# Kernel optimization log

Measured on AMD Instinct MI355X. Metric: run time of the kernel, lower is better.

The kernel has to match this reference:

```python
import jax, jax.numpy as jnp
import numpy as np

DIM = 256
NUM_HEADS = 8
HEAD_DIM = DIM // NUM_HEADS
WINDOW = 256
STRIDE = 192  # int(256 * (1 - 0.25))
HIDDEN = int(DIM * 4.0)
EPS_IN = 1e-5


def setup_inputs() -> dict:
    key = jax.random.key(0)
    ks = jax.random.split(key, 10)
    B, C, L = 4, DIM, 8192
    s = lambda fan_in: 1.0 / np.sqrt(fan_in)
    return {
        "x": jax.random.normal(ks[0], (B, C, L), jnp.float32),
        "pos": jax.random.normal(ks[1], (1, C, 1), jnp.float32),
        "w_qkv": jax.random.normal(ks[2], (3 * C, C), jnp.float32) * s(C),
        "b_qkv": jax.random.normal(ks[3], (3 * C,), jnp.float32) * s(C),
        "w_out": jax.random.normal(ks[4], (C, C), jnp.float32) * s(C),
        "b_out": jax.random.normal(ks[5], (C,), jnp.float32) * s(C),
        "w_mlp1": jax.random.normal(ks[6], (HIDDEN, C), jnp.float32) * s(C),
        "b_mlp1": jax.random.normal(ks[7], (HIDDEN,), jnp.float32) * s(C),
        "w_mlp2": jax.random.normal(ks[8], (C, HIDDEN), jnp.float32) * s(HIDDEN),
        "b_mlp2": jax.random.normal(ks[9], (C,), jnp.float32) * s(HIDDEN),
    }


def conv1x1(x, w, b):
    # x: (B, Cin, L), w: (Cout, Cin), b: (Cout,)
    return jnp.einsum("oc,bcl->bol", w, x) + b[None, :, None]


def instance_norm(x, eps=EPS_IN):
    # InstanceNorm1d, affine=False: normalize each (B, C) row over L (biased var)
    mean = jnp.mean(x, axis=-1, keepdims=True)
    var = jnp.var(x, axis=-1, keepdims=True)
    return (x - mean) * jax.lax.rsqrt(var + eps)


def reference(x, pos, w_qkv, b_qkv, w_out, b_out, w_mlp1, b_mlp1, w_mlp2, b_mlp2):
    B, C, L = x.shape
    residual = x
    xp = x + pos
    qkv = conv1x1(xp, w_qkv, b_qkv)  # (B, 3C, L)
    q, k, v = jnp.split(qkv, 3, axis=1)
    # (B, H, L, hd)
    to_heads = lambda t: t.reshape(B, NUM_HEADS, HEAD_DIM, L).transpose(0, 1, 3, 2)
    q, k, v = to_heads(q), to_heads(k), to_heads(v)

    # static overlapping window index map
    starts = np.arange(0, L, STRIDE)                      # (nW,)
    idx = starts[:, None] + np.arange(WINDOW)[None, :]     # (nW, W)
    valid = idx < L                                        # (nW, W)
    idxc = np.minimum(idx, L - 1)
    valid_j = jnp.asarray(valid)

    qw = q[:, :, idxc, :]  # (B, H, nW, W, hd)
    kw = k[:, :, idxc, :]
    vw = v[:, :, idxc, :]
    scale = HEAD_DIM ** -0.5
    scores = jnp.einsum("bhnqd,bhnkd->bhnqk", qw, kw) * scale
    scores = jnp.where(valid_j[None, None, :, None, :], scores, -jnp.inf)
    attn = jax.nn.softmax(scores, axis=-1)
    win_out = jnp.einsum("bhnqk,bhnkd->bhnqd", attn, vw)
    win_out = win_out * valid_j[None, None, :, :, None]

    # overlap-add scatter + count normalization
    flat_idx = idxc.reshape(-1)
    out = jnp.zeros_like(q).at[:, :, flat_idx, :].add(
        win_out.reshape(B, NUM_HEADS, -1, HEAD_DIM))
    counts = jnp.zeros((L,), x.dtype).at[flat_idx].add(
        valid_j.reshape(-1).astype(x.dtype))
    out = out / jnp.clip(counts, 1e-8)[None, None, :, None]

    attn_out = out.transpose(0, 1, 3, 2).reshape(B, C, L)
    y = conv1x1(attn_out, w_out, b_out) + residual
    y = instance_norm(y)

    # AttentionMLP1D: conv1x1 -> GELU -> conv1x1 -> InstanceNorm, + residual
    h = jax.nn.gelu(conv1x1(y, w_mlp1, b_mlp1), approximate=False)
    m = instance_norm(conv1x1(h, w_mlp2, b_mlp2))
    return m + y
```

## Files before the change

### kernel.cpp

```cpp
#include <hip/hip_runtime.h>
#include <hip/hip_bf16.h>
#include <math.h>

#define B_   4
#define C_   256
#define L_   8192
#define NH   8
#define HD   32
#define WIN  256
#define STR  192
#define NWIN 43
#define HID  1024

typedef short short8 __attribute__((ext_vector_type(8)));
typedef float f32x4  __attribute__((ext_vector_type(4)));

typedef __attribute__((address_space(3))) unsigned int       as3_u32;
typedef __attribute__((address_space(1))) const unsigned int as1_u32;

__device__ __forceinline__ void gll16(const void* g, void* l) {
    __builtin_amdgcn_global_load_lds((as1_u32*)g, (as3_u32*)l, 16, 0, 0);
}

__device__ __forceinline__ short f2b(float f) {
    unsigned u = __builtin_bit_cast(unsigned, f);
    u += 0x7fffu + ((u >> 16) & 1u);
    return (short)(u >> 16);
}
__device__ __forceinline__ float b2f(short s) {
    return __builtin_bit_cast(float, (unsigned)((unsigned short)s) << 16);
}
__device__ __forceinline__ unsigned pk2(float a, float b) {
    return (unsigned)(unsigned short)f2b(a) | ((unsigned)(unsigned short)f2b(b) << 16);
}
__device__ __forceinline__ float gelu_exact(float v) {
    return 0.5f * v * (1.0f + erff(v * 0.70710678118654752f));
}

template<int MODE>
__global__ __launch_bounds__(256)
void mgemm(const short* __restrict__ Wb, const short* __restrict__ Xsrc,
           const float* __restrict__ bias, const float* __restrict__ resid,
           void* __restrict__ outp)
{
    constexpr int K = (MODE == 3) ? 1024 : 256;
    constexpr int M = (MODE == 0) ? 768 : (MODE == 2) ? 1024 : 256;
    constexpr int LDSZ = (MODE == 0 || MODE == 2) ? 34816 : 32768;
    __shared__ __align__(16) char lds[LDSZ];

    const int t    = threadIdx.x;
    const int lane = t & 63, wid = t >> 6;
    const int wm   = wid >> 1, wn = wid & 1;
    const int b    = blockIdx.z;
    const int o0   = blockIdx.y * 128;
    const int l0   = blockIdx.x * 128;
    const int l15  = lane & 15, kb = lane >> 4;

    f32x4 acc[4][4] = {};
    const short* Xb = Xsrc + (size_t)b * L_ * K;

    int pn1[4], pj1[4]; bool ptwo[4];
    if constexpr (MODE == 1) {
        #pragma unroll
        for (int it = 0; it < 4; ++it) {
            int r = (it * 256 + t) >> 3;
            int l = l0 + r;
            int n1 = l / STR;
            pn1[it] = n1; pj1[it] = l - n1 * STR;
            ptwo[it] = (n1 >= 1) && (pj1[it] < WIN - STR);
        }
    }

    for (int c0 = 0; c0 < K; c0 += 64) {
        __syncthreads();
        #pragma unroll
        for (int it = 0; it < 4; ++it) {
            int d = it * 256 + t;
            int r = d >> 3, pc = d & 7;
            int clog = pc ^ (r & 7);
            gll16(Wb + (size_t)(o0 + r) * K + c0 + clog * 8,
                  lds + (it * 256 + wid * 64) * 16);
        }
        if constexpr (MODE == 1) {
            #pragma unroll
            for (int it = 0; it < 4; ++it) {
                int d = it * 256 + t;
                int r = d >> 3, pc = d & 7;
                int clog = pc ^ (r & 7);
                int c = c0 + clog * 8;
                int h = c >> 5, dd = c & 31;
                size_t base = ((((size_t)(b * NH + h)) * NWIN + pn1[it]) * WIN + pj1[it]) * HD + dd;
                short8 vv = *(const short8*)&Xsrc[base];
                if (ptwo[it]) {
                    short8 u = *(const short8*)&Xsrc[base - 2048];
                    #pragma unroll
                    for (int e = 0; e < 8; ++e) vv[e] = f2b(b2f(vv[e]) + b2f(u[e]));
                }
                *(short8*)(lds + 16384 + d * 16) = vv;
            }
        } else {
            #pragma unroll
            for (int it = 0; it < 4; ++it) {
                int d = it * 256 + t;
                int r = d >> 3, pc = d & 7;
                int clog = pc ^ (r & 7);
                gll16(Xb + (size_t)(l0 + r) * K + c0 + clog * 8,
                      lds + 16384 + (it * 256 + wid * 64) * 16);
            }
        }
        __syncthreads();
        #pragma unroll
        for (int kk = 0; kk < 2; ++kk) {
            short8 af[4], bf[4];
            #pragma unroll
            for (int i = 0; i < 4; ++i)
                af[i] = *(const short8*)(lds +
                    ((wm * 64 + i * 16 + l15) * 8 + ((kk * 4 + kb) ^ (l15 & 7))) * 16);
            #pragma unroll
            for (int j = 0; j < 4; ++j)
                bf[j] = *(const short8*)(lds + 16384 +
                    ((wn * 64 + j * 16 + l15) * 8 + ((kk * 4 + kb) ^ (l15 & 7))) * 16);
            #pragma unroll
            for (int i = 0; i < 4; ++i)
                #pragma unroll
                for (int j = 0; j < 4; ++j)
                    acc[i][j] = __builtin_amdgcn_mfma_f32_16x16x32_bf16(af[i], bf[j], acc[i][j], 0, 0, 0);
        }
    }

    const int orow = (lane >> 4) * 4;

    if constexpr (MODE == 1 || MODE == 3) {
        float* out = (float*)outp;
        #pragma unroll
        for (int i = 0; i < 4; ++i) {
            #pragma unroll
            for (int r = 0; r < 4; ++r) {
                const int o = o0 + wm * 64 + i * 16 + orow + r;
                const float bv = bias[o];
                #pragma unroll
                for (int j = 0; j < 4; ++j) {
                    const int l = l0 + wn * 64 + j * 16 + l15;
                    float v = acc[i][j][r] + bv;
                    if (MODE == 1) v += resid[((size_t)b * C_ + o) * L_ + l];
                    out[((size_t)b * M + o) * L_ + l] = v;
                }
            }
        }
    } else {
        __syncthreads();
        short* Ts = (short*)lds;
        const float qscale = (MODE == 0 && o0 < 256) ? 0.17677669529663687f : 1.0f;
        #pragma unroll
        for (int i = 0; i < 4; ++i) {
            #pragma unroll
            for (int r = 0; r < 4; ++r) {
                const int ol = wm * 64 + i * 16 + orow + r;
                const float bv = bias[o0 + ol];
                #pragma unroll
                for (int j = 0; j < 4; ++j) {
                    const int ll = wn * 64 + j * 16 + l15;
                    float v = acc[i][j][r] + bv;
                    if (MODE == 2) v = gelu_exact(v);
                    if (MODE == 0) v *= qscale;
                    Ts[ll * 136 + ol] = f2b(v);
                }
            }
        }
        __syncthreads();
        if constexpr (MODE == 2) {
            short* ht = (short*)outp;
            #pragma unroll
            for (int it = 0; it < 8; ++it) {
                int idx = t + it * 256;
                int ll = idx >> 4, ck = (idx & 15) * 8;
                short8 v = *(const short8*)(Ts + ll * 136 + ck);
                *(short8*)(ht + ((size_t)b * L_ + l0 + ll) * HID + o0 + ck) = v;
            }
        } else {
            short* qkv = (short*)outp;
            #pragma unroll
            for (int it = 0; it < 8; ++it) {
                int idx = t + it * 256;
                int hb = idx >> 9, rem = idx & 511;
                int ll = rem >> 2, dk = (rem & 3) * 8;
                short8 v = *(const short8*)(Ts + ll * 136 + hb * 32 + dk);
                int og = o0 + hb * 32;
                int part = og >> 8, h = (og & 255) >> 5;
                short* dst = qkv + (size_t)part * ((size_t)B_ * NH * L_ * HD)
                           + (((size_t)(b * NH + h) * L_ + l0 + ll) * HD + dk);
                *(short8*)dst = v;
            }
        }
    }
}

__global__ __launch_bounds__(256)
void attn_k(const short* __restrict__ q, const short* __restrict__ k,
            const short* __restrict__ v, short* __restrict__ win_out)
{
    __shared__ __align__(16) short Kl[256][40];
    __shared__ __align__(16) short Vt[32][264];
    __shared__ __align__(16) short Pl[4][64][40];

    const int n = blockIdx.x, h = blockIdx.y, b = blockIdx.z;
    const int start = n * STR;
    const int t = threadIdx.x;
    const int lane = t & 63, w = t >> 6;
    const int l15 = lane & 15, kb = lane >> 4;
    const size_t hbase = (size_t)(b * NH + h) * L_ * HD;

    {
        int l = start + t; if (l > L_ - 1) l = L_ - 1;
        const short8* gk = (const short8*)&k[hbase + (size_t)l * HD];
        const short8* gv = (const short8*)&v[hbase + (size_t)l * HD];
        short8 k0 = gk[0], k1 = gk[1], k2 = gk[2], k3 = gk[3];
        short8 v0 = gv[0], v1 = gv[1], v2 = gv[2], v3 = gv[3];
        *(short8*)&Kl[t][0]  = k0; *(short8*)&Kl[t][8]  = k1;
        *(short8*)&Kl[t][16] = k2; *(short8*)&Kl[t][24] = k3;
        #pragma unroll
        for (int e = 0; e < 8; ++e) {
            Vt[e][t]      = v0[e];
            Vt[8 + e][t]  = v1[e];
            Vt[16 + e][t] = v2[e];
            Vt[24 + e][t] = v3[e];
        }
    }

    short8 qf[4];
    #pragma unroll
    for (int j = 0; j < 4; ++j) {
        int lq = start + w * 64 + j * 16 + l15; if (lq > L_ - 1) lq = L_ - 1;
        qf[j] = *(const short8*)&q[hbase + (size_t)lq * HD + kb * 8];
    }
    __syncthreads();

    const bool domask = (start + WIN > L_);
    f32x4 ot[2][4] = {};
    float ls[4] = {};
    const f32x4 zacc = {};

    for (int kt = 0; kt < 8; ++kt) {
        short8 ka[2];
        #pragma unroll
        for (int i = 0; i < 2; ++i)
            ka[i] = *(const short8*)&Kl[kt * 32 + i * 16 + l15][kb * 8];
        f32x4 st[2][4];
        #pragma unroll
        for (int i = 0; i < 2; ++i)
            #pragma unroll
            for (int j = 0; j < 4; ++j)
                st[i][j] = __builtin_amdgcn_mfma_f32_16x16x32_bf16(ka[i], qf[j], zacc, 0, 0, 0);

        if (domask) {
            #pragma unroll
            for (int i = 0; i < 2; ++i)
                #pragma unroll
                for (int r = 0; r < 4; ++r) {
                    int kp = start + kt * 32 + i * 16 + kb * 4 + r;
                    if (kp >= L_) {
                        #pragma unroll
                        for (int j = 0; j < 4; ++j) st[i][j][r] = -1e30f;
                    }
                }
        }

        #pragma unroll
        for (int j = 0; j < 4; ++j) {
            #pragma unroll
            for (int i = 0; i < 2; ++i) {
                float p0 = __expf(st[i][j][0]);
                float p1 = __expf(st[i][j][1]);
                float p2 = __expf(st[i][j][2]);
                float p3 = __expf(st[i][j][3]);
                ls[j] += (p0 + p1) + (p2 + p3);
                uint2 u;
                u.x = pk2(p0, p1);
                u.y = pk2(p2, p3);
                *(uint2*)&Pl[w][j * 16 + l15][i * 16 + kb * 4] = u;
            }
        }
        asm volatile("s_waitcnt lgkmcnt(0)" ::: "memory");
        __builtin_amdgcn_sched_barrier(0);

        short8 pb[4], va[2];
        #pragma unroll
        for (int j = 0; j < 4; ++j)
            pb[j] = *(const short8*)&Pl[w][j * 16 + l15][kb * 8];
        #pragma unroll
        for (int i = 0; i < 2; ++i)
            va[i] = *(const short8*)&Vt[i * 16 + l15][kt * 32 + kb * 8];
        #pragma unroll
        for (int i = 0; i < 2; ++i)
            #pragma unroll
            for (int j = 0; j < 4; ++j)
                ot[i][j] = __builtin_amdgcn_mfma_f32_16x16x32_bf16(va[i], pb[j], ot[i][j], 0, 0, 0);
    }

    float sc[4];
    #pragma unroll
    for (int j = 0; j < 4; ++j) {
        float s = ls[j];
        s += __shfl_xor(s, 16);
        s += __shfl_xor(s, 32);
        int lq = start + w * 64 + j * 16 + l15;
        int nhi = lq / STR;
        int nlo = (lq >= WIN) ? ((lq - WIN) / STR + 1) : 0;
        sc[j] = 1.0f / (s * (float)(nhi - nlo + 1));
    }

    short* base = win_out + (((size_t)(b * NH + h) * NWIN + n) * WIN) * HD;
    #pragma unroll
    for (int i = 0; i < 2; ++i)
        #pragma unroll
        for (int j = 0; j < 4; ++j) {
            int qrow = w * 64 + j * 16 + l15;
            int d    = i * 16 + kb * 4;
            f32x4 o = ot[i][j];
            uint2 u;
            u.x = pk2(o[0] * sc[j], o[1] * sc[j]);
            u.y = pk2(o[2] * sc[j], o[3] * sc[j]);
            *(uint2*)&base[(size_t)qrow * HD + d] = u;
        }
}

__global__ __launch_bounds__(256)
void stats_k(const float* __restrict__ src, float2* __restrict__ stt)
{
    const int row = blockIdx.x;
    const float* s = src + (size_t)row * L_;
    const int t = threadIdx.x;
    float sum = 0.f, ssq = 0.f;
    #pragma unroll
    for (int i = 0; i < 8; ++i) {
        float4 vv = *(const float4*)&s[t * 4 + i * 1024];
        sum += (vv.x + vv.y) + (vv.z + vv.w);
        ssq += vv.x*vv.x + vv.y*vv.y + vv.z*vv.z + vv.w*vv.w;
    }
    #pragma unroll
    for (int off = 32; off > 0; off >>= 1) {
        sum += __shfl_down(sum, off);
        ssq += __shfl_down(ssq, off);
    }
    __shared__ float rbuf[8];
    if ((t & 63) == 0) { rbuf[t >> 6] = sum; rbuf[4 + (t >> 6)] = ssq; }
    __syncthreads();
    if (t == 0) {
        float a  = (rbuf[0] + rbuf[1]) + (rbuf[2] + rbuf[3]);
        float q2 = (rbuf[4] + rbuf[5]) + (rbuf[6] + rbuf[7]);
        float mean = a * (1.0f / L_);
        float var  = q2 * (1.0f / L_) - mean * mean;
        stt[row] = make_float2(mean, rsqrtf(var + 1e-5f));
    }
}

__global__ __launch_bounds__(256)
void prep_k(const float* __restrict__ in, const float* __restrict__ pos,
            const float2* __restrict__ stt, short* __restrict__ outT)
{
    __shared__ float T[64][65];
    const int b = blockIdx.z, c0 = blockIdx.y * 64, l0 = blockIdx.x * 64;
    const int t = threadIdx.x;
    #pragma unroll
    for (int it = 0; it < 4; ++it) {
        int idx = t + it * 256;
        int c = idx >> 4, l4 = (idx & 15) * 4;
        float4 v = *(const float4*)&in[((size_t)b * C_ + c0 + c) * L_ + l0 + l4];
        if (stt) {
            float2 ms = stt[b * C_ + c0 + c];
            v.x = (v.x - ms.x) * ms.y; v.y = (v.y - ms.x) * ms.y;
            v.z = (v.z - ms.x) * ms.y; v.w = (v.w - ms.x) * ms.y;
        }
        float p = pos ? pos[c0 + c] : 0.f;
        T[c][l4 + 0] = v.x + p; T[c][l4 + 1] = v.y + p;
        T[c][l4 + 2] = v.z + p; T[c][l4 + 3] = v.w + p;
    }
    __syncthreads();
    #pragma unroll
    for (int it = 0; it < 2; ++it) {
        int idx = t + it * 256;
        int l = idx >> 3, ck = (idx & 7) * 8;
        short8 o;
        #pragma unroll
        for (int j = 0; j < 8; ++j) o[j] = f2b(T[ck + j][l]);
        *(short8*)&outT[((size_t)b * L_ + l0 + l) * C_ + c0 + ck] = o;
    }
}

__global__ __launch_bounds__(256)
void wconv_k(const float* a, const float* b, const float* c, const float* d,
             short* oa, short* ob, short* oc, short* od)
{
    int i = (blockIdx.x * 256 + threadIdx.x) * 8;
    const float* s; short* o; int off;
    if (i < 196608)      { s = a; o = oa; off = i; }
    else if (i < 262144) { s = b; o = ob; off = i - 196608; }
    else if (i < 524288) { s = c; o = oc; off = i - 262144; }
    else                 { s = d; o = od; off = i - 524288; }
    float4 v0 = *(const float4*)(s + off);
    float4 v1 = *(const float4*)(s + off + 4);
    short8 r;
    r[0] = f2b(v0.x); r[1] = f2b(v0.y); r[2] = f2b(v0.z); r[3] = f2b(v0.w);
    r[4] = f2b(v1.x); r[5] = f2b(v1.y); r[6] = f2b(v1.z); r[7] = f2b(v1.w);
    *(short8*)(o + off) = r;
}

__global__ __launch_bounds__(256)
void norm_k(const float* __restrict__ src, const float* __restrict__ add,
            const float2* __restrict__ ast, float* __restrict__ dst)
{
    const int row = blockIdx.x;
    const float* s = src + (size_t)row * L_;
    const int t = threadIdx.x;
    float4 vals[8];
    float sum = 0.f, ssq = 0.f;
    #pragma unroll
    for (int i = 0; i < 8; ++i) {
        float4 vv = *(const float4*)&s[t * 4 + i * 1024];
        vals[i] = vv;
        sum += (vv.x + vv.y) + (vv.z + vv.w);
        ssq += vv.x*vv.x + vv.y*vv.y + vv.z*vv.z + vv.w*vv.w;
    }
    #pragma unroll
    for (int off = 32; off > 0; off >>= 1) {
        sum += __shfl_down(sum, off);
        ssq += __shfl_down(ssq, off);
    }
    __shared__ float rbuf[8];
    __shared__ float s_mean, s_rstd;
    if ((t & 63) == 0) { rbuf[t >> 6] = sum; rbuf[4 + (t >> 6)] = ssq; }
    __syncthreads();
    if (t == 0) {
        float a  = (rbuf[0] + rbuf[1]) + (rbuf[2] + rbuf[3]);
        float q2 = (rbuf[4] + rbuf[5]) + (rbuf[6] + rbuf[7]);
        float mean = a * (1.0f / L_);
        float var  = q2 * (1.0f / L_) - mean * mean;
        s_mean = mean;
        s_rstd = rsqrtf(var + 1e-5f);
    }
    __syncthreads();
    const float mean = s_mean, rstd = s_rstd;
    const float2 ms = ast[row];
    float* d = dst + (size_t)row * L_;
    const float* ar = add + (size_t)row * L_;
    #pragma unroll
    for (int i = 0; i < 8; ++i) {
        float4 vv = vals[i];
        float4 av = *(const float4*)&ar[t * 4 + i * 1024];
        vv.x = (vv.x - mean) * rstd + (av.x - ms.x) * ms.y;
        vv.y = (vv.y - mean) * rstd + (av.y - ms.x) * ms.y;
        vv.z = (vv.z - mean) * rstd + (av.z - ms.x) * ms.y;
        vv.w = (vv.w - mean) * rstd + (av.w - ms.x) * ms.y;
        *(float4*)&d[t * 4 + i * 1024] = vv;
    }
}

extern "C" void kernel_launch(void* const* d_in, const int* in_sizes, int n_in,
                              void* d_out, int out_size, void* d_ws, size_t ws_size,
                              hipStream_t stream) {
    const float* x      = (const float*)d_in[0];
    const float* pos    = (const float*)d_in[1];
    const float* w_qkv  = (const float*)d_in[2];
    const float* b_qkv  = (const float*)d_in[3];
    const float* w_out  = (const float*)d_in[4];
    const float* b_out  = (const float*)d_in[5];
    const float* w_mlp1 = (const float*)d_in[6];
    const float* b_mlp1 = (const float*)d_in[7];
    const float* w_mlp2 = (const float*)d_in[8];
    const float* b_mlp2 = (const float*)d_in[9];
    float* out = (float*)d_out;

    constexpr size_t MB = 1u << 20;
    char* w = (char*)d_ws;
    short*  xp_t  = (short*)(w);
    short*  qb    = (short*)(w + 16 * MB);
    short*  winb  = (short*)(w + 64 * MB);
    float*  yb    = (float*)(w + 88 * MB);
    short*  y_t   = (short*)(w + 120 * MB);
    short*  h_t   = (short*)(w);
    float2* yst   = (float2*)(w + 136 * MB);
    short*  wqb   = (short*)(w + 137 * MB);
    short*  wob   = wqb + 196608;
    short*  wm1b  = wob + 65536;
    short*  wm2b  = wm1b + 262144;

    const size_t SZ = (size_t)B_ * C_ * L_;

    wconv_k<<<384, 256, 0, stream>>>(w_qkv, w_out, w_mlp1, w_mlp2, wqb, wob, wm1b, wm2b);
    prep_k <<<dim3(128, 4, B_), 256, 0, stream>>>(x, pos, nullptr, xp_t);

    mgemm<0><<<dim3(64, 6, B_), 256, 0, stream>>>(wqb, xp_t, b_qkv, nullptr, qb);
    attn_k  <<<dim3(NWIN, NH, B_), 256, 0, stream>>>(qb, qb + SZ, qb + 2 * SZ, winb);
    mgemm<1><<<dim3(64, 2, B_), 256, 0, stream>>>(wob, winb, b_out, x, yb);
    stats_k <<<B_ * C_, 256, 0, stream>>>(yb, yst);
    prep_k  <<<dim3(128, 4, B_), 256, 0, stream>>>(yb, nullptr, yst, y_t);
    mgemm<2><<<dim3(64, 8, B_), 256, 0, stream>>>(wm1b, y_t, b_mlp1, nullptr, h_t);
    mgemm<3><<<dim3(64, 2, B_), 256, 0, stream>>>(wm2b, h_t, b_mlp2, nullptr, out);
    norm_k  <<<B_ * C_, 256, 0, stream>>>(out, yb, yst, out);
}
```

Baseline: 205.3 us.

## Keep activation tile in registers and loop over output tiles with double-buffered weights

The GEMM kernel is restructured so that each block owns a 128-column L tile and keeps its activation operand in registers across all output-channel tiles. Weight tiles of 128x256 are streamed into a double-buffered 128 KB LDS area, with the next tile prefetched while MFMAs run. The grid shrinks to 64xB blocks with launch_bounds(256,1), trading parallelism and occupancy (only 256 blocks) for reuse of the activation operand. The exact erf GELU is also replaced by a tanh-style sigmoid approximation, which changes numerics slightly.

```diff
diff --git a/kernel.cpp b/kernel.cpp
--- a/kernel.cpp
+++ b/kernel.cpp
@@ -33,164 +33,171 @@
 __device__ __forceinline__ unsigned pk2(float a, float b) {
     return (unsigned)(unsigned short)f2b(a) | ((unsigned)(unsigned short)f2b(b) << 16);
 }
-__device__ __forceinline__ float gelu_exact(float v) {
-    return 0.5f * v * (1.0f + erff(v * 0.70710678118654752f));
+__device__ __forceinline__ float gelu_fast(float x) {
+    float t = x * x;
+    float u = fmaf(0.0713548162726f * t, x, 1.59576912161f * x);
+    return x * __frcp_rn(1.0f + __expf(-u));
 }
 
 template<int MODE>
-__global__ __launch_bounds__(256)
-void mgemm(const short* __restrict__ Wb, const short* __restrict__ Xsrc,
-           const float* __restrict__ bias, const float* __restrict__ resid,
-           void* __restrict__ outp)
+__global__ __launch_bounds__(256, 1)
+void wsg(const short* __restrict__ Wb, const short* __restrict__ Xsrc,
+         const float* __restrict__ bias, const float* __restrict__ resid,
+         void* __restrict__ outp)
 {
-    constexpr int K = (MODE == 3) ? 1024 : 256;
-    constexpr int M = (MODE == 0) ? 768 : (MODE == 2) ? 1024 : 256;
-    constexpr int LDSZ = (MODE == 0 || MODE == 2) ? 34816 : 32768;
-    __shared__ __align__(16) char lds[LDSZ];
+    constexpr int K   = (MODE == 3) ? 1024 : 256;
+    constexpr int M   = (MODE == 0) ? 768 : (MODE == 2) ? 1024 : 256;
+    constexpr int NOT = M / 128;
+    constexpr int NKO = K / 256;
+    constexpr int TOT = NOT * NKO;
+
+    __shared__ __align__(16) short lds[2][32768];
 
     const int t    = threadIdx.x;
     const int lane = t & 63, wid = t >> 6;
-    const int wm   = wid >> 1, wn = wid & 1;
-    const int b    = blockIdx.z;
-    const int o0   = blockIdx.y * 128;
+    const int wo   = wid >> 1, wl = wid & 1;
+    const int b    = blockIdx.y;
     const int l0   = blockIdx.x * 128;
     const int l15  = lane & 15, kb = lane >> 4;
-
-    f32x4 acc[4][4] = {};
-    const short* Xb = Xsrc + (size_t)b * L_ * K;
-
-    int pn1[4], pj1[4]; bool ptwo[4];
-    if constexpr (MODE == 1) {
-        #pragma unroll
-        for (int it = 0; it < 4; ++it) {
-            int r = (it * 256 + t) >> 3;
-            int l = l0 + r;
-            int n1 = l / STR;
-            pn1[it] = n1; pj1[it] = l - n1 * STR;
-            ptwo[it] = (n1 >= 1) && (pj1[it] < WIN - STR);
-        }
-    }
-
-    for (int c0 = 0; c0 < K; c0 += 64) {
-        __syncthreads();
-        #pragma unroll
-        for (int it = 0; it < 4; ++it) {
-            int d = it * 256 + t;
-            int r = d >> 3, pc = d & 7;
-            int clog = pc ^ (r & 7);
-            gll16(Wb + (size_t)(o0 + r) * K + c0 + clog * 8,
-                  lds + (it * 256 + wid * 64) * 16);
-        }
-        if constexpr (MODE == 1) {
-            #pragma unroll
-            for (int it = 0; it < 4; ++it) {
-                int d = it * 256 + t;
-                int r = d >> 3, pc = d & 7;
-                int clog = pc ^ (r & 7);
-                int c = c0 + clog * 8;
-                int h = c >> 5, dd = c & 31;
-                size_t base = ((((size_t)(b * NH + h)) * NWIN + pn1[it]) * WIN + pj1[it]) * HD + dd;
-                short8 vv = *(const short8*)&Xsrc[base];
-                if (ptwo[it]) {
-                    short8 u = *(const short8*)&Xsrc[base - 2048];
+    const int orow = kb * 4;
+
+    short8 bf[(MODE == 3) ? 2 : 1][4][8];
+
+    auto loadB = [&](short8 (*dst)[8], int ko) {
+        #pragma unroll
+        for (int j = 0; j < 4; ++j) {
+            const int l = l0 + wl * 64 + j * 16 + l15;
+            if constexpr (MODE == 1) {
+                const int n1 = l / STR, j1 = l - (l / STR) * STR;
+                const bool two = (n1 >= 1) && (j1 < WIN - STR);
+                #pragma unroll
+                for (int kk = 0; kk < 8; ++kk) {
+                    const int h = kk, dd = kb * 8;
+                    size_t base = ((((size_t)(b * NH + h)) * NWIN + n1) * WIN + j1) * HD + dd;
+                    short8 vv = *(const short8*)&Xsrc[base];
+                    if (two) {
+                        short8 u = *(const short8*)&Xsrc[base - 2048];
+                        #pragma unroll
+                        for (int e = 0; e < 8; ++e) vv[e] = f2b(b2f(vv[e]) + b2f(u[e]));
+                    }
+                    dst[j][kk] = vv;
+                }
+            } else {
+                #pragma unroll
+                for (int kk = 0; kk < 8; ++kk)
+                    dst[j][kk] = *(const short8*)&Xsrc[(size_t)(b * L_ + l) * K
+                                                       + ko * 256 + kk * 32 + kb * 8];
+            }
+        }
+    };
+
+    auto stageA = [&](int ot, int ko, int buf) {
+        #pragma unroll
+        for (int it = 0; it < 16; ++it) {
+            int dl = it * 256 + t;
+            int r = dl >> 5, d = dl & 31;
+            int clog = d ^ (r & 7);
+            gll16(Wb + (size_t)(ot * 128 + r) * K + ko * 256 + clog * 8,
+                  &lds[buf][dl * 8]);
+        }
+    };
+
+    loadB(bf[0], 0);
+    stageA(0, 0, 0);
+    __syncthreads();
+
+    int cur = 0;
+    #pragma unroll 1
+    for (int ot = 0; ot < NOT; ++ot) {
+        f32x4 acc[4][4] = {};
+        #pragma unroll
+        for (int ko = 0; ko < NKO; ++ko) {
+            const int q = ot * NKO + ko + 1;
+            if (q < TOT) stageA(q / NKO, q % NKO, cur ^ 1);
+            if constexpr (MODE == 3) {
+                if (q < TOT) loadB(bf[(ko + 1) & 1], q % NKO);
+            }
+            #pragma unroll
+            for (int kk = 0; kk < 8; ++kk) {
+                short8 af[4];
+                #pragma unroll
+                for (int i = 0; i < 4; ++i)
+                    af[i] = *(const short8*)&lds[cur][(wo * 64 + i * 16 + l15) * 256
+                                + (((kk * 4 + kb) ^ (l15 & 7)) * 8)];
+                #pragma unroll
+                for (int i = 0; i < 4; ++i)
                     #pragma unroll
-                    for (int e = 0; e < 8; ++e) vv[e] = f2b(b2f(vv[e]) + b2f(u[e]));
+                    for (int j = 0; j < 4; ++j)
+                        acc[i][j] = __builtin_amdgcn_mfma_f32_16x16x32_bf16(
+                            af[i], bf[(MODE == 3) ? (ko & 1) : 0][j][kk], acc[i][j], 0, 0, 0);
+            }
+            __syncthreads();
+            cur ^= 1;
+        }
+
+        const int o0 = ot * 128;
+        if constexpr (MODE == 1 || MODE == 3) {
+            float* out = (float*)outp;
+            #pragma unroll
+            for (int i = 0; i < 4; ++i) {
+                #pragma unroll
+                for (int r = 0; r < 4; ++r) {
+                    const int o = o0 + wo * 64 + i * 16 + orow + r;
+                    const float bv = bias[o];
+                    #pragma unroll
+                    for (int j = 0; j < 4; ++j) {
+                        const int l = l0 + wl * 64 + j * 16 + l15;
+                        float v = acc[i][j][r] + bv;
+                        if (MODE == 1) v += resid[((size_t)b * C_ + o) * L_ + l];
+                        out[((size_t)b * M + o) * L_ + l] = v;
+                    }
                 }
-                *(short8*)(lds + 16384 + d * 16) = vv;
             }
         } else {
-            #pragma unroll
-            for (int it = 0; it < 4; ++it) {
-                int d = it * 256 + t;
-                int r = d >> 3, pc = d & 7;
-                int clog = pc ^ (r & 7);
-                gll16(Xb + (size_t)(l0 + r) * K + c0 + clog * 8,
-                      lds + 16384 + (it * 256 + wid * 64) * 16);
-            }
-        }
-        __syncthreads();
-        #pragma unroll
-        for (int kk = 0; kk < 2; ++kk) {
-            short8 af[4], bf[4];
-            #pragma unroll
-            for (int i = 0; i < 4; ++i)
-                af[i] = *(const short8*)(lds +
-                    ((wm * 64 + i * 16 + l15) * 8 + ((kk * 4 + kb) ^ (l15 & 7))) * 16);
-            #pragma unroll
-            for (int j = 0; j < 4; ++j)
-                bf[j] = *(const short8*)(lds + 16384 +
-                    ((wn * 64 + j * 16 + l15) * 8 + ((kk * 4 + kb) ^ (l15 & 7))) * 16);
-            #pragma unroll
-            for (int i = 0; i < 4; ++i)
-                #pragma unroll
-                for (int j = 0; j < 4; ++j)
-                    acc[i][j] = __builtin_amdgcn_mfma_f32_16x16x32_bf16(af[i], bf[j], acc[i][j], 0, 0, 0);
-        }
-    }
-
-    const int orow = (lane >> 4) * 4;
-
-    if constexpr (MODE == 1 || MODE == 3) {
-        float* out = (float*)outp;
-        #pragma unroll
-        for (int i = 0; i < 4; ++i) {
-            #pragma unroll
-            for (int r = 0; r < 4; ++r) {
-                const int o = o0 + wm * 64 + i * 16 + orow + r;
-                const float bv = bias[o];
-                #pragma unroll
-                for (int j = 0; j < 4; ++j) {
-                    const int l = l0 + wn * 64 + j * 16 + l15;
-                    float v = acc[i][j][r] + bv;
-                    if (MODE == 1) v += resid[((size_t)b * C_ + o) * L_ + l];
-                    out[((size_t)b * M + o) * L_ + l] = v;
+            short* Ts = &lds[cur ^ 1][0];
+            const float qscale = (MODE == 0 && o0 < 256) ? 0.17677669529663687f : 1.0f;
+            #pragma unroll
+            for (int i = 0; i < 4; ++i) {
+                #pragma unroll
+                for (int r = 0; r < 4; ++r) {
+                    const int ol = wo * 64 + i * 16 + orow + r;
+                    const float bv = bias[o0 + ol];
+                    #pragma unroll
+                    for (int j = 0; j < 4; ++j) {
+                        const int ll = wl * 64 + j * 16 + l15;
+                        float v = acc[i][j][r] + bv;
+                        if (MODE == 2) v = gelu_fast(v);
+                        if (MODE == 0) v *= qscale;
+                        Ts[ll * 136 + ol] = f2b(v);
+                    }
                 }
             }
-        }
-    } else {
-        __syncthreads();
-        short* Ts = (short*)lds;
-        const float qscale = (MODE == 0 && o0 < 256) ? 0.17677669529663687f : 1.0f;
-        #pragma unroll
-        for (int i = 0; i < 4; ++i) {
-            #pragma unroll
-            for (int r = 0; r < 4; ++r) {
-                const int ol = wm * 64 + i * 16 + orow + r;
-                const float bv = bias[o0 + ol];
-                #pragma unroll
-                for (int j = 0; j < 4; ++j) {
-                    const int ll = wn * 64 + j * 16 + l15;
-                    float v = acc[i][j][r] + bv;
-                    if (MODE == 2) v = gelu_exact(v);
-                    if (MODE == 0) v *= qscale;
-                    Ts[ll * 136 + ol] = f2b(v);
+            __syncthreads();
+            if constexpr (MODE == 2) {
+                short* ht = (short*)outp;
+                #pragma unroll
+                for (int it = 0; it < 8; ++it) {
+                    int idx = t + it * 256;
+                    int ll = idx >> 4, ck = (idx & 15) * 8;
+                    short8 v = *(const short8*)(Ts + ll * 136 + ck);
+                    *(short8*)(ht + ((size_t)b * L_ + l0 + ll) * HID + o0 + ck) = v;
                 }
-            }
-        }
-        __syncthreads();
-        if constexpr (MODE == 2) {
-            short* ht = (short*)outp;
-            #pragma unroll
-            for (int it = 0; it < 8; ++it) {
-                int idx = t + it * 256;
-                int ll = idx >> 4, ck = (idx & 15) * 8;
-                short8 v = *(const short8*)(Ts + ll * 136 + ck);
-                *(short8*)(ht + ((size_t)b * L_ + l0 + ll) * HID + o0 + ck) = v;
-            }
-        } else {
-            short* qkv = (short*)outp;
-            #pragma unroll
-            for (int it = 0; it < 8; ++it) {
-                int idx = t + it * 256;
-                int hb = idx >> 9, rem = idx & 511;
-                int ll = rem >> 2, dk = (rem & 3) * 8;
-                short8 v = *(const short8*)(Ts + ll * 136 + hb * 32 + dk);
-                int og = o0 + hb * 32;
-                int part = og >> 8, h = (og & 255) >> 5;
-                short* dst = qkv + (size_t)part * ((size_t)B_ * NH * L_ * HD)
-                           + (((size_t)(b * NH + h) * L_ + l0 + ll) * HD + dk);
-                *(short8*)dst = v;
-            }
+            } else {
+                short* qkv = (short*)outp;
+                #pragma unroll
+                for (int it = 0; it < 8; ++it) {
+                    int idx = t + it * 256;
+                    int hb = idx >> 9, rem = idx & 511;
+                    int ll = rem >> 2, dk = (rem & 3) * 8;
+                    short8 v = *(const short8*)(Ts + ll * 136 + hb * 32 + dk);
+                    int og = o0 + hb * 32;
+                    int part = og >> 8, h = (og & 255) >> 5;
+                    short* dst = qkv + (size_t)part * ((size_t)B_ * NH * L_ * HD)
+                               + (((size_t)(b * NH + h) * L_ + l0 + ll) * HD + dk);
+                    *(short8*)dst = v;
+                }
+            }
+            __syncthreads();
         }
     }
 }
@@ -489,12 +496,12 @@
     wconv_k<<<384, 256, 0, stream>>>(w_qkv, w_out, w_mlp1, w_mlp2, wqb, wob, wm1b, wm2b);
     prep_k <<<dim3(128, 4, B_), 256, 0, stream>>>(x, pos, nullptr, xp_t);
 
-    mgemm<0><<<dim3(64, 6, B_), 256, 0, stream>>>(wqb, xp_t, b_qkv, nullptr, qb);
-    attn_k  <<<dim3(NWIN, NH, B_), 256, 0, stream>>>(qb, qb + SZ, qb + 2 * SZ, winb);
-    mgemm<1><<<dim3(64, 2, B_), 256, 0, stream>>>(wob, winb, b_out, x, yb);
-    stats_k <<<B_ * C_, 256, 0, stream>>>(yb, yst);
-    prep_k  <<<dim3(128, 4, B_), 256, 0, stream>>>(yb, nullptr, yst, y_t);
-    mgemm<2><<<dim3(64, 8, B_), 256, 0, stream>>>(wm1b, y_t, b_mlp1, nullptr, h_t);
-    mgemm<3><<<dim3(64, 2, B_), 256, 0, stream>>>(wm2b, h_t, b_mlp2, nullptr, out);
-    norm_k  <<<B_ * C_, 256, 0, stream>>>(out, yb, yst, out);
-}
+    wsg<0><<<dim3(64, B_), 256, 0, stream>>>(wqb, xp_t, b_qkv, nullptr, qb);
+    attn_k <<<dim3(NWIN, NH, B_), 256, 0, stream>>>(qb, qb + SZ, qb + 2 * SZ, winb);
+    wsg<1><<<dim3(64, B_), 256, 0, stream>>>(wob, winb, b_out, x, yb);
+    stats_k<<<B_ * C_, 256, 0, stream>>>(yb, yst);
+    prep_k <<<dim3(128, 4, B_), 256, 0, stream>>>(yb, nullptr, yst, y_t);
+    wsg<2><<<dim3(64, B_), 256, 0, stream>>>(wm1b, y_t, b_mlp1, nullptr, h_t);
+    wsg<3><<<dim3(64, B_), 256, 0, stream>>>(wm2b, h_t, b_mlp2, nullptr, out);
+    norm_k <<<B_ * C_, 256, 0, stream>>>(out, yb, yst, out);
+}
```

Result: slower. 313.5 us (+52.7%).
